# Performance work log

Hardware: AMD Instinct MI355X
Metric: run time of the kernel (lower is better)

Reference implementation:

```python
import jax, jax.numpy as jnp
import numpy as np

KS = 3               # kernel_size
PAD = (KS - 1) // 2  # same padding
K2 = KS * KS
B, H, W = 4, 1024, 1024
SCALE = 1.0          # residual scale


def setup_inputs() -> dict:
    key = jax.random.key(0)
    k1, k2, k3 = jax.random.split(key, 3)
    init_dem = jax.random.normal(k1, (B, 1, H, W), jnp.float32)
    weight = jax.random.normal(k2, (B, K2, H, W), jnp.float32)          # modulation mask
    offset = jax.random.normal(k3, (B, 2 * K2, H, W), jnp.float32) * 2.0  # (dy,dx) per tap
    w = jnp.ones((1, 1, KS, KS), jnp.float32)   # nn.Parameter ones
    b = jnp.zeros((1,), jnp.float32)            # nn.Parameter zeros
    return {"init_dem": init_dem, "weight": weight, "offset": offset, "w": w, "b": b}


def _bilinear(img, y, x):
    # img: [H, W]; y, x: [H, W] fractional sample positions. Zero padding outside.
    Hh, Ww = img.shape
    y0 = jnp.floor(y)
    x0 = jnp.floor(x)

    def gather(yi, xi):
        valid = (yi >= 0) & (yi <= Hh - 1) & (xi >= 0) & (xi <= Ww - 1)
        yc = jnp.clip(yi, 0, Hh - 1).astype(jnp.int32)
        xc = jnp.clip(xi, 0, Ww - 1).astype(jnp.int32)
        return jnp.where(valid, img[yc, xc], 0.0)

    wy1 = y - y0
    wx1 = x - x0
    wy0 = 1.0 - wy1
    wx0 = 1.0 - wx1
    return (wy0 * wx0 * gather(y0, x0)
            + wy0 * wx1 * gather(y0, x0 + 1.0)
            + wy1 * wx0 * gather(y0 + 1.0, x0)
            + wy1 * wx1 * gather(y0 + 1.0, x0 + 1.0))


def reference(init_dem, weight, offset, w, b):
    # residual=True branch: zero-mean normalize the modulation mask over taps
    mask = weight - jnp.mean(weight, axis=1, keepdims=True)            # [B, K2, H, W]
    off = offset.reshape(B, K2, 2, H, W)                               # (dy, dx) per tap

    ky, kx = jnp.meshgrid(jnp.arange(KS), jnp.arange(KS), indexing="ij")
    ky = ky.reshape(-1).astype(jnp.float32)                            # [K2]
    kx = kx.reshape(-1).astype(jnp.float32)
    hh = jnp.arange(H, dtype=jnp.float32)[:, None]                     # [H, 1]
    ww = jnp.arange(W, dtype=jnp.float32)[None, :]                     # [1, W]

    # sample position for tap k at output pixel (h, w): p = p0 + k - pad + offset
    ys = (hh - PAD + ky[:, None, None])[None] + off[:, :, 0]           # [B, K2, H, W]
    xs = (ww - PAD + kx[:, None, None])[None] + off[:, :, 1]

    # vmap over batch (image varies) and taps (image shared)
    sample = jax.vmap(jax.vmap(_bilinear, in_axes=(None, 0, 0)),
                      in_axes=(0, 0, 0))(init_dem[:, 0], ys, xs)       # [B, K2, H, W]

    refined = jnp.einsum("bkhw,k->bhw", sample * mask, w.reshape(-1)) + b[0]
    return refined[:, None] + SCALE * init_dem                          # residual add
```

## Files before the change

kernel.cpp:

```cpp
#include <hip/hip_runtime.h>

#define BB 4
#define HH 1024
#define WW 1024
#define K2 9
#define PAD 1

#define R   12
#define TW  64
#define TH  16
#define RW  (TW + 2*R)
#define RH  (TH + 2*R)
#define RSZ (RW * RH)

__global__ __launch_bounds__(256) void dcn_kernel(
    const float* __restrict__ init_dem,
    const float* __restrict__ weight,
    const float* __restrict__ offset,
    const float* __restrict__ wk,
    const float* __restrict__ bias,
    float* __restrict__ out)
{
    __shared__ float region[RSZ];

    const int HW = HH * WW;

    int i    = blockIdx.x;
    int b    = (i & 7) >> 1;
    int widx = ((i >> 3) << 1) | (i & 1);
    int tile_w = widx & 15;
    int tile_h = widx >> 4;
    int w0 = tile_w * TW;
    int h0 = tile_h * TH;

    const float* img = init_dem + (size_t)b * HW;

    int tid = threadIdx.x;
#pragma unroll
    for (int it = 0; it < (RSZ + 255) / 256; ++it) {
        int e = tid + it * 256;
        if (e < RSZ) {
            int r = e / RW;
            int c = e - r * RW;
            int gy = h0 - R + r;
            int gx = w0 - R + c;
            float v = 0.f;
            if ((unsigned)gy < (unsigned)HH && (unsigned)gx < (unsigned)WW)
                v = img[gy * WW + gx];
            region[e] = v;
        }
    }
    __syncthreads();

    const int tx = tid & 63;
    const int ty = tid >> 6;
    const float bval = bias[0];

    float wgt[K2];
#pragma unroll
    for (int k = 0; k < K2; ++k) wgt[k] = wk[k];

#pragma unroll 2
    for (int p = 0; p < 4; ++p) {
        int h = h0 + ty + p * 4;
        int w = w0 + tx;
        int rem = h * WW + w;

        const float* wq = weight + (size_t)b * K2 * HW + rem;
        const float* oq = offset + (size_t)b * 2 * K2 * HW + rem;

        float wt[K2], dy[K2], dx[K2];
        float wsum = 0.f;
#pragma unroll
        for (int k = 0; k < K2; ++k) {
            wt[k] = __builtin_nontemporal_load(wq + (size_t)k * HW);
            dy[k] = __builtin_nontemporal_load(oq + (size_t)(2 * k) * HW);
            dx[k] = __builtin_nontemporal_load(oq + (size_t)(2 * k + 1) * HW);
            wsum += wt[k];
        }
        const float mean = wsum * (1.0f / K2);

        const float fy = (float)(ty + p * 4 + R - PAD);
        const float fx = (float)(tx + R - PAD);

        float acc = 0.f;
#pragma unroll
        for (int k = 0; k < K2; ++k) {
            const int ky = k / 3, kx = k % 3;

            float ysl = (fy + (float)ky) + dy[k];
            float xsl = (fx + (float)kx) + dx[k];

            float y0f = floorf(ysl);
            float x0f = floorf(xsl);
            float wy1 = ysl - y0f;
            float wx1 = xsl - x0f;
            float wy0 = 1.f - wy1;
            float wx0 = 1.f - wx1;

            int y0l = (int)y0f;
            int x0l = (int)x0f;

            float v00, v01, v10, v11;
            if (((unsigned)y0l < (unsigned)(RH - 1)) &
                ((unsigned)x0l < (unsigned)(RW - 1))) {
                int base = y0l * RW + x0l;
                v00 = region[base];
                v10 = region[base + RW];
                v01 = region[base + 1];
                v11 = region[base + RW + 1];
            } else {
                int y0g = y0l + (h0 - R);
                int x0g = x0l + (w0 - R);
                int y1g = y0g + 1;
                int x1g = x0g + 1;
                bool y0v = (y0g >= 0) & (y0g < HH);
                bool y1v = (y1g >= 0) & (y1g < HH);
                bool x0v = (x0g >= 0) & (x0g < WW);
                bool x1v = (x1g >= 0) & (x1g < WW);
                int yc0 = min(max(y0g, 0), HH - 1);
                int yc1 = min(max(y1g, 0), HH - 1);
                int xc0 = min(max(x0g, 0), WW - 1);
                int xc1 = min(max(x1g, 0), WW - 1);
                v00 = (y0v & x0v) ? img[(size_t)yc0 * WW + xc0] : 0.f;
                v01 = (y0v & x1v) ? img[(size_t)yc0 * WW + xc1] : 0.f;
                v10 = (y1v & x0v) ? img[(size_t)yc1 * WW + xc0] : 0.f;
                v11 = (y1v & x1v) ? img[(size_t)yc1 * WW + xc1] : 0.f;
            }

            float samp = wy0 * (wx0 * v00 + wx1 * v01)
                       + wy1 * (wx0 * v10 + wx1 * v11);
            acc += samp * (wt[k] - mean) * wgt[k];
        }

        float resid = region[(ty + p * 4 + R) * RW + (tx + R)];
        float rres  = acc + bval + resid;
        __builtin_nontemporal_store(rres, out + (size_t)b * HW + rem);
    }
}

extern "C" void kernel_launch(void* const* d_in, const int* in_sizes, int n_in,
                              void* d_out, int out_size, void* d_ws, size_t ws_size,
                              hipStream_t stream) {
    const float* init_dem = (const float*)d_in[0];
    const float* weight   = (const float*)d_in[1];
    const float* offset   = (const float*)d_in[2];
    const float* wk       = (const float*)d_in[3];
    const float* bias     = (const float*)d_in[4];
    float* out            = (float*)d_out;

    const int nblocks = BB * (WW / TW) * (HH / TH);
    dcn_kernel<<<dim3(nblocks), dim3(256), 0, stream>>>(init_dem, weight, offset, wk, bias, out);
}
```

Baseline: 105.6 us.

## Double-buffer weight/offset streams into LDS via async global_load_lds

Streams the 27 per-pixel weight and offset planes directly into a double-buffered LDS staging area using global_load_lds, prefetching the next row batch while the current one is computed and waiting with explicit vmcnt counts. The mask mean is folded algebraically so the taps are processed in a single pass with two accumulators, without first summing the weights. This is meant to hide global memory latency and cut register pressure. The cost is about 55KB of extra LDS per block, which lowers occupancy, and correctness now depends on hand-written waitcnt accounting with no barrier, relying on each wave reading only the slots it loaded itself.

```diff
diff --git a/kernel.cpp b/kernel.cpp
--- a/kernel.cpp
+++ b/kernel.cpp
@@ -13,6 +13,15 @@
 #define RH  (TH + 2*R)
 #define RSZ (RW * RH)
 
+#define NSLOT  27
+#define SBUF_N (NSLOT * 256)
+
+__device__ __forceinline__ void gload_lds(const float* g, float* l) {
+    __builtin_amdgcn_global_load_lds((const __attribute__((address_space(1))) void*)g,
+                                     (__attribute__((address_space(3))) void*)l,
+                                     4, 0, 0);
+}
+
 __global__ __launch_bounds__(256) void dcn_kernel(
     const float* __restrict__ init_dem,
     const float* __restrict__ weight,
@@ -22,6 +31,7 @@
     float* __restrict__ out)
 {
     __shared__ float region[RSZ];
+    __shared__ float sbuf[2 * SBUF_N];
 
     const int HW = HH * WW;
 
@@ -34,8 +44,32 @@
     int h0 = tile_h * TH;
 
     const float* img = init_dem + (size_t)b * HW;
+    const float* wbase = weight + (size_t)b * K2 * HW;
+    const float* obase = offset + (size_t)b * 2 * K2 * HW;
 
-    int tid = threadIdx.x;
+    const int tid  = threadIdx.x;
+    const int tx   = tid & 63;
+    const int wv   = tid >> 6;
+
+    float wgt[K2];
+#pragma unroll
+    for (int k = 0; k < K2; ++k) wgt[k] = wk[k];
+    const float bval = bias[0];
+
+#define ISSUE_BATCH(P, BF) do {                                                   \
+        int rem_ = (h0 + wv + (P) * 4) * WW + w0 + tx;                            \
+        const float* wq_ = wbase + rem_;                                          \
+        const float* oq_ = obase + rem_;                                          \
+        _Pragma("unroll")                                                         \
+        for (int kk = 0; kk < K2; ++kk) {                                         \
+            gload_lds(wq_ + (size_t)kk * HW,           &sbuf[(BF) * SBUF_N + ((3 * kk + 0) * 4 + wv) * 64]); \
+            gload_lds(oq_ + (size_t)(2 * kk) * HW,     &sbuf[(BF) * SBUF_N + ((3 * kk + 1) * 4 + wv) * 64]); \
+            gload_lds(oq_ + (size_t)(2 * kk + 1) * HW, &sbuf[(BF) * SBUF_N + ((3 * kk + 2) * 4 + wv) * 64]); \
+        }                                                                         \
+    } while (0)
+
+    ISSUE_BATCH(0, 0);
+
 #pragma unroll
     for (int it = 0; it < (RSZ + 255) / 256; ++it) {
         int e = tid + it * 256;
@@ -52,44 +86,38 @@
     }
     __syncthreads();
 
-    const int tx = tid & 63;
-    const int ty = tid >> 6;
-    const float bval = bias[0];
+    const float fx = (float)(tx + R - PAD);
 
-    float wgt[K2];
-#pragma unroll
-    for (int k = 0; k < K2; ++k) wgt[k] = wk[k];
+    for (int p = 0; p < 4; ++p) {
+        if (p == 0)      ISSUE_BATCH(1, 1);
+        else if (p == 1) ISSUE_BATCH(2, 0);
+        else if (p == 2) ISSUE_BATCH(3, 1);
 
-#pragma unroll 2
-    for (int p = 0; p < 4; ++p) {
-        int h = h0 + ty + p * 4;
-        int w = w0 + tx;
-        int rem = h * WW + w;
+        if (p > 0) {
+            if (p < 3) asm volatile("s_waitcnt vmcnt(27)" ::: "memory");
+            else       asm volatile("s_waitcnt vmcnt(0)"  ::: "memory");
+        }
 
-        const float* wq = weight + (size_t)b * K2 * HW + rem;
-        const float* oq = offset + (size_t)b * 2 * K2 * HW + rem;
+        const float* sb = &sbuf[(p & 1) * SBUF_N];
+        const int h   = h0 + wv + p * 4;
+        const int rem = h * WW + w0 + tx;
+        const float fy = (float)(wv + p * 4 + R - PAD);
 
-        float wt[K2], dy[K2], dx[K2];
-        float wsum = 0.f;
-#pragma unroll
-        for (int k = 0; k < K2; ++k) {
-            wt[k] = __builtin_nontemporal_load(wq + (size_t)k * HW);
-            dy[k] = __builtin_nontemporal_load(oq + (size_t)(2 * k) * HW);
-            dx[k] = __builtin_nontemporal_load(oq + (size_t)(2 * k + 1) * HW);
-            wsum += wt[k];
-        }
-        const float mean = wsum * (1.0f / K2);
+        float accA = 0.f;
+        float accB = 0.f;
+        float msum = 0.f;
 
-        const float fy = (float)(ty + p * 4 + R - PAD);
-        const float fx = (float)(tx + R - PAD);
-
-        float acc = 0.f;
 #pragma unroll
         for (int k = 0; k < K2; ++k) {
             const int ky = k / 3, kx = k % 3;
 
-            float ysl = (fy + (float)ky) + dy[k];
-            float xsl = (fx + (float)kx) + dx[k];
+            float wtv = sb[((3 * k + 0) * 4 + wv) * 64 + tx];
+            float dyv = sb[((3 * k + 1) * 4 + wv) * 64 + tx];
+            float dxv = sb[((3 * k + 2) * 4 + wv) * 64 + tx];
+            msum += wtv;
+
+            float ysl = (fy + (float)ky) + dyv;
+            float xsl = (fx + (float)kx) + dxv;
 
             float y0f = floorf(ysl);
             float x0f = floorf(xsl);
@@ -130,13 +158,16 @@
 
             float samp = wy0 * (wx0 * v00 + wx1 * v01)
                        + wy1 * (wx0 * v10 + wx1 * v11);
-            acc += samp * (wt[k] - mean) * wgt[k];
+            float sw = samp * wgt[k];
+            accA += sw * wtv;
+            accB += sw;
         }
 
-        float resid = region[(ty + p * 4 + R) * RW + (tx + R)];
-        float rres  = acc + bval + resid;
+        float resid = region[(wv + p * 4 + R) * RW + (tx + R)];
+        float rres  = accA - msum * (1.0f / K2) * accB + bval + resid;
         __builtin_nontemporal_store(rres, out + (size_t)b * HW + rem);
     }
+#undef ISSUE_BATCH
 }
 
 extern "C" void kernel_launch(void* const* d_in, const int* in_sizes, int n_in,
```

New measurement: 221.8 us. 110% more time.
